# Kernel optimization log

Measured on AMD Instinct MI355X. Metric: run time of the kernel, lower is better.

Reference implementation:

```python
import jax, jax.numpy as jnp
import numpy as np

EPS = 1e-5

def _sage(x, src, dst, counts, w_msg, w_root, b, n_nodes):
    # mean-aggregate neighbor features (src -> dst), then linear
    msgs = x[src]                                             # [E, D]
    summed = jax.ops.segment_sum(msgs, dst, num_segments=n_nodes)
    mean = summed / counts                                    # [N, D]
    return mean @ w_msg + x @ w_root + b

def _layernorm(x, gamma, beta):
    mu = jnp.mean(x, axis=-1, keepdims=True)
    var = jnp.var(x, axis=-1, keepdims=True)
    return (x - mu) * jax.lax.rsqrt(var + EPS) * gamma + beta

def setup_inputs() -> dict:
    key = jax.random.key(0)
    N, E, D = 100000, 1600000, 128
    ks = jax.random.split(key, 20)
    z = jax.random.normal(ks[0], (N, D), dtype=jnp.float32)
    edge_index = jax.random.randint(ks[1], (2, E), 0, N, dtype=jnp.int32)
    def lin(k, din, dout):
        return jax.random.normal(k, (din, dout), dtype=jnp.float32) / np.sqrt(din)
    params = {
        'w_msg1': lin(ks[2], 128, 256), 'w_root1': lin(ks[3], 128, 256),
        'b1': jnp.zeros((256,), jnp.float32),
        'g1': jax.random.uniform(ks[4], (256,), jnp.float32, 0.9, 1.1),
        'beta1': jax.random.normal(ks[5], (256,), jnp.float32) * 0.05,
        'w_msg2': lin(ks[6], 256, 256), 'w_root2': lin(ks[7], 256, 256),
        'b2': jnp.zeros((256,), jnp.float32),
        'g2': jax.random.uniform(ks[8], (256,), jnp.float32, 0.9, 1.1),
        'beta2': jax.random.normal(ks[9], (256,), jnp.float32) * 0.05,
        'w_msg3': lin(ks[10], 256, 128), 'w_root3': lin(ks[11], 256, 128),
        'b3': jnp.zeros((128,), jnp.float32),
        'g3': jax.random.uniform(ks[12], (128,), jnp.float32, 0.9, 1.1),
        'beta3': jax.random.normal(ks[13], (128,), jnp.float32) * 0.05,
        'w_msg4': lin(ks[14], 128, 9), 'w_root4': lin(ks[15], 128, 9),
        'b4': jnp.zeros((9,), jnp.float32),
    }
    return {'z': z, 'edge_index': edge_index, **params}

def reference(z, edge_index,
              w_msg1, w_root1, b1, g1, beta1,
              w_msg2, w_root2, b2, g2, beta2,
              w_msg3, w_root3, b3, g3, beta3,
              w_msg4, w_root4, b4):
    N = z.shape[0]
    src, dst = edge_index[0], edge_index[1]
    counts = jax.ops.segment_sum(jnp.ones_like(dst, dtype=z.dtype), dst, num_segments=N)
    counts = jnp.maximum(counts, 1.0)[:, None]
    x = jax.nn.relu(_layernorm(_sage(z, src, dst, counts, w_msg1, w_root1, b1, N), g1, beta1))
    x = jax.nn.relu(_layernorm(_sage(x, src, dst, counts, w_msg2, w_root2, b2, N), g2, beta2))
    x = jax.nn.relu(_layernorm(_sage(x, src, dst, counts, w_msg3, w_root3, b3, N), g3, beta3))
    x = _sage(x, src, dst, counts, w_msg4, w_root4, b4, N)
    return x
```

## Files before the change

### kernel.cpp

```cpp
#include <hip/hip_runtime.h>
#include <hip/hip_bf16.h>


#define EPS 1e-5f

typedef unsigned short u16;
typedef short bf16x8_t __attribute__((ext_vector_type(8)));
typedef float f32x4_t __attribute__((ext_vector_type(4)));

__device__ inline unsigned int bfpack(float a, float b) {
    unsigned int ua = __builtin_bit_cast(unsigned int, a);
    unsigned int ub = __builtin_bit_cast(unsigned int, b);
    ua += 0x7fffu + ((ua >> 16) & 1u);
    ub += 0x7fffu + ((ub >> 16) & 1u);
    return (ua >> 16) | (ub & 0xffff0000u);
}

__device__ inline u16 bfr(float a) {
    unsigned int u = __builtin_bit_cast(unsigned int, a);
    u += 0x7fffu + ((u >> 16) & 1u);
    return (u16)(u >> 16);
}

__device__ inline float bf2f(u16 v) {
    unsigned int u = ((unsigned int)v) << 16;
    return __builtin_bit_cast(float, u);
}

__device__ inline float bflo(unsigned int q) { return __builtin_bit_cast(float, q << 16); }
__device__ inline float bfhi(unsigned int q) { return __builtin_bit_cast(float, q & 0xffff0000u); }

#define ACC8(A, Q)                                         \
    A[0] += bflo(Q.x); A[1] += bfhi(Q.x);                  \
    A[2] += bflo(Q.y); A[3] += bfhi(Q.y);                  \
    A[4] += bflo(Q.z); A[5] += bfhi(Q.z);                  \
    A[6] += bflo(Q.w); A[7] += bfhi(Q.w);

__global__ __launch_bounds__(256) void zero_f4(float4* __restrict__ p, int n4) {
    int i = blockIdx.x * 256 + threadIdx.x;
    if (i < n4) p[i] = make_float4(0.f, 0.f, 0.f, 0.f);
}

__global__ __launch_bounds__(256) void cast_bf16(const float* __restrict__ x,
                                                 u16* __restrict__ y, int n4) {
    int i = blockIdx.x * 256 + threadIdx.x;
    if (i >= n4) return;
    float4 v = ((const float4*)x)[i];
    ((uint2*)y)[i] = make_uint2(bfpack(v.x, v.y), bfpack(v.z, v.w));
}

struct WtJobs {
    const float* W[6];
    u16* WT[6];
    int K[6], N[6];
};
__global__ __launch_bounds__(256) void transpose_cast6(WtJobs jobs) {
    int j = blockIdx.y;
    int idx = blockIdx.x * 256 + threadIdx.x;
    int K = jobs.K[j], Nn = jobs.N[j];
    if (idx >= K * Nn) return;
    int k = idx / Nn, n = idx - k * Nn;
    jobs.WT[j][(long)n * K + k] = bfr(jobs.W[j][idx]);
}

__global__ __launch_bounds__(256) void count_deg(const int* __restrict__ dst,
                                                 int* __restrict__ deg, int E) {
    int e = blockIdx.x * 256 + threadIdx.x;
    if (e < E) atomicAdd(&deg[dst[e]], 1);
}

__global__ __launch_bounds__(256) void partial_sums(const int* __restrict__ deg,
                                                    int* __restrict__ partials, int N) {
    __shared__ int lds[4];
    int tid = threadIdx.x;
    int base = blockIdx.x * 1024 + tid * 4;
    int s = 0;
    if (base + 3 < N) {
        int4 v = *(const int4*)(deg + base);
        s = v.x + v.y + v.z + v.w;
    } else {
        for (int i = 0; i < 4; ++i)
            if (base + i < N) s += deg[base + i];
    }
#pragma unroll
    for (int m = 32; m >= 1; m >>= 1) s += __shfl_xor(s, m);
    if ((tid & 63) == 0) lds[tid >> 6] = s;
    __syncthreads();
    if (tid == 0) partials[blockIdx.x] = lds[0] + lds[1] + lds[2] + lds[3];
}

__global__ __launch_bounds__(256) void scan_partials(int* __restrict__ partials, int nb) {
    __shared__ int lds[256];
    int tid = threadIdx.x;
    int v = (tid < nb) ? partials[tid] : 0;
    lds[tid] = v;
    __syncthreads();
    for (int off = 1; off < 256; off <<= 1) {
        int t = (tid >= off) ? lds[tid - off] : 0;
        __syncthreads();
        lds[tid] += t;
        __syncthreads();
    }
    if (tid < nb) partials[tid] = lds[tid] - v;
}

__global__ __launch_bounds__(256) void write_rowptr(const int* __restrict__ deg,
                                                    const int* __restrict__ partials,
                                                    int* __restrict__ rowptr,
                                                    int* __restrict__ cursor,
                                                    float* __restrict__ inv, int N, int E) {
    __shared__ int lds[256];
    int tid = threadIdx.x;
    int base = blockIdx.x * 1024 + tid * 4;
    int d[4];
    int s = 0;
#pragma unroll
    for (int i = 0; i < 4; ++i) {
        d[i] = (base + i < N) ? deg[base + i] : 0;
        s += d[i];
    }
    lds[tid] = s;
    __syncthreads();
    for (int off = 1; off < 256; off <<= 1) {
        int t = (tid >= off) ? lds[tid - off] : 0;
        __syncthreads();
        lds[tid] += t;
        __syncthreads();
    }
    int run = partials[blockIdx.x] + lds[tid] - s;
#pragma unroll
    for (int i = 0; i < 4; ++i) {
        int idx = base + i;
        if (idx < N) {
            rowptr[idx] = run;
            cursor[idx] = run;
            inv[idx] = 1.0f / fmaxf((float)d[i], 1.0f);
            run += d[i];
        }
    }
    if (blockIdx.x == 0 && tid == 0) rowptr[N] = E;
}

__global__ __launch_bounds__(256) void fill_csr_range(const int* __restrict__ src,
                                                      const int* __restrict__ dst,
                                                      int* __restrict__ cursor,
                                                      int* __restrict__ eidx, int E,
                                                      int lo, int bs) {
    int e = blockIdx.x * 256 + threadIdx.x;
    if (e >= E) return;
    int d = dst[e];
    if ((unsigned)(d - lo) < (unsigned)bs) {
        int p = atomicAdd(&cursor[d], 1);
        eidx[p] = src[e];
    }
}

__global__ __launch_bounds__(256) void gather_scale256(const u16* __restrict__ x,
                                                       const int* __restrict__ rowptr,
                                                       const int* __restrict__ eidx,
                                                       const float* __restrict__ inv,
                                                       u16* __restrict__ agg, int N) {
    int wave = threadIdx.x >> 6;
    int lane = threadIdx.x & 63;
    int half = lane >> 5;
    int sub = lane & 31;
    int row = blockIdx.x * 4 + wave;
    if (row >= N) return;
    int beg = rowptr[row], end = rowptr[row + 1];
    float a[8] = {}, b[8] = {};
    int j = beg + half;
    for (; j + 2 < end; j += 4) {
        uint4 q0 = *(const uint4*)(x + (long)eidx[j] * 256 + sub * 8);
        uint4 q1 = *(const uint4*)(x + (long)eidx[j + 2] * 256 + sub * 8);
        ACC8(a, q0);
        ACC8(b, q1);
    }
    if (j < end) {
        uint4 q = *(const uint4*)(x + (long)eidx[j] * 256 + sub * 8);
        ACC8(a, q);
    }
#pragma unroll
    for (int i = 0; i < 8; ++i) {
        a[i] += b[i];
        a[i] += __shfl_xor(a[i], 32);
    }
    if (half == 0) {
        float s = inv[row];
        uint4 o;
        o.x = bfpack(a[0] * s, a[1] * s);
        o.y = bfpack(a[2] * s, a[3] * s);
        o.z = bfpack(a[4] * s, a[5] * s);
        o.w = bfpack(a[6] * s, a[7] * s);
        *(uint4*)(agg + (long)row * 256 + sub * 8) = o;
    }
}

__global__ __launch_bounds__(256) void gather_scale128(const u16* __restrict__ x,
                                                       const int* __restrict__ rowptr,
                                                       const int* __restrict__ eidx,
                                                       const float* __restrict__ inv,
                                                       u16* __restrict__ agg, int N) {
    int wave = threadIdx.x >> 6;
    int lane = threadIdx.x & 63;
    int quarter = lane >> 4;
    int sub = lane & 15;
    int row = blockIdx.x * 4 + wave;
    if (row >= N) return;
    int beg = rowptr[row], end = rowptr[row + 1];
    float a[8] = {}, b[8] = {};
    int j = beg + quarter;
    for (; j + 4 < end; j += 8) {
        uint4 q0 = *(const uint4*)(x + (long)eidx[j] * 128 + sub * 8);
        uint4 q1 = *(const uint4*)(x + (long)eidx[j + 4] * 128 + sub * 8);
        ACC8(a, q0);
        ACC8(b, q1);
    }
    if (j < end) {
        uint4 q = *(const uint4*)(x + (long)eidx[j] * 128 + sub * 8);
        ACC8(a, q);
    }
#pragma unroll
    for (int i = 0; i < 8; ++i) {
        a[i] += b[i];
        a[i] += __shfl_xor(a[i], 16);
        a[i] += __shfl_xor(a[i], 32);
    }
    if (quarter == 0) {
        float s = inv[row];
        uint4 o;
        o.x = bfpack(a[0] * s, a[1] * s);
        o.y = bfpack(a[2] * s, a[3] * s);
        o.z = bfpack(a[4] * s, a[5] * s);
        o.w = bfpack(a[6] * s, a[7] * s);
        *(uint4*)(agg + (long)row * 128 + sub * 8) = o;
    }
}

__global__ __launch_bounds__(256) void gather_add_ln_relu128(const u16* __restrict__ y,
                                                             const int* __restrict__ rowptr,
                                                             const int* __restrict__ eidx,
                                                             const float* __restrict__ inv,
                                                             const u16* __restrict__ r,
                                                             const float* __restrict__ g,
                                                             const float* __restrict__ be,
                                                             u16* __restrict__ out, int N) {
    int wave = threadIdx.x >> 6;
    int lane = threadIdx.x & 63;
    int quarter = lane >> 4;
    int sub = lane & 15;
    int row = blockIdx.x * 4 + wave;
    if (row >= N) return;
    int beg = rowptr[row], end = rowptr[row + 1];
    float a[8] = {}, b[8] = {};
    int j = beg + quarter;
    for (; j + 4 < end; j += 8) {
        uint4 q0 = *(const uint4*)(y + (long)eidx[j] * 128 + sub * 8);
        uint4 q1 = *(const uint4*)(y + (long)eidx[j + 4] * 128 + sub * 8);
        ACC8(a, q0);
        ACC8(b, q1);
    }
    if (j < end) {
        uint4 q = *(const uint4*)(y + (long)eidx[j] * 128 + sub * 8);
        ACC8(a, q);
    }
#pragma unroll
    for (int i = 0; i < 8; ++i) {
        a[i] += b[i];
        a[i] += __shfl_xor(a[i], 16);
        a[i] += __shfl_xor(a[i], 32);
    }
    float iv = inv[row];
    uint4 rr = *(const uint4*)(r + (long)row * 128 + sub * 8);
    float v[8];
    v[0] = a[0] * iv + bflo(rr.x); v[1] = a[1] * iv + bfhi(rr.x);
    v[2] = a[2] * iv + bflo(rr.y); v[3] = a[3] * iv + bfhi(rr.y);
    v[4] = a[4] * iv + bflo(rr.z); v[5] = a[5] * iv + bfhi(rr.z);
    v[6] = a[6] * iv + bflo(rr.w); v[7] = a[7] * iv + bfhi(rr.w);
    float s = 0.f, ss = 0.f;
#pragma unroll
    for (int i = 0; i < 8; ++i) { s += v[i]; ss += v[i] * v[i]; }
#pragma unroll
    for (int m = 8; m >= 1; m >>= 1) {
        s += __shfl_xor(s, m);
        ss += __shfl_xor(ss, m);
    }
    float mean = s / 128.f;
    float var = ss / 128.f - mean * mean;
    float rs = rsqrtf(var + EPS);
    if (quarter == 0) {
        int col = sub * 8;
        float4 g0 = *(const float4*)&g[col];
        float4 g1 = *(const float4*)&g[col + 4];
        float4 e0 = *(const float4*)&be[col];
        float4 e1 = *(const float4*)&be[col + 4];
        float o0 = fmaxf((v[0] - mean) * rs * g0.x + e0.x, 0.f);
        float o1 = fmaxf((v[1] - mean) * rs * g0.y + e0.y, 0.f);
        float o2 = fmaxf((v[2] - mean) * rs * g0.z + e0.z, 0.f);
        float o3 = fmaxf((v[3] - mean) * rs * g0.w + e0.w, 0.f);
        float o4 = fmaxf((v[4] - mean) * rs * g1.x + e1.x, 0.f);
        float o5 = fmaxf((v[5] - mean) * rs * g1.y + e1.y, 0.f);
        float o6 = fmaxf((v[6] - mean) * rs * g1.z + e1.z, 0.f);
        float o7 = fmaxf((v[7] - mean) * rs * g1.w + e1.w, 0.f);
        uint4 o;
        o.x = bfpack(o0, o1);
        o.y = bfpack(o2, o3);
        o.z = bfpack(o4, o5);
        o.w = bfpack(o6, o7);
        *(uint4*)(out + (long)row * 128 + sub * 8) = o;
    }
}

__global__ __launch_bounds__(256) void gather9_final(const u16* __restrict__ y,
                                                     const int* __restrict__ rowptr,
                                                     const int* __restrict__ eidx,
                                                     const float* __restrict__ inv,
                                                     const float* __restrict__ r,
                                                     float* __restrict__ out, int N) {
    int idx = blockIdx.x * 256 + threadIdx.x;
    int row = idx >> 4;
    int c = idx & 15;
    if (row >= N || c >= 9) return;
    int beg = rowptr[row], end = rowptr[row + 1];
    float a = 0.f;
    for (int j = beg; j < end; ++j) a += bf2f(y[(long)eidx[j] * 9 + c]);
    out[(long)row * 9 + c] = a * inv[row] + r[(long)row * 9 + c];
}

__global__ __launch_bounds__(256) void mfma_gemm_wide_ln(const u16* A1,
                                                         const u16* __restrict__ A2,
                                                         const u16* __restrict__ WT1,
                                                         const u16* __restrict__ WT2,
                                                         const float* __restrict__ bias,
                                                         const float* __restrict__ g,
                                                         const float* __restrict__ be,
                                                         u16* out, int M, int K) {
    __shared__ __align__(16) u16 smem[64 * 260];
    u16* As = smem;
    u16* Ws = smem + 64 * 40;
    const int tid = threadIdx.x;
    const int bm = blockIdx.x * 64;
    const int l = tid & 63;
    const int w = tid >> 6;
    const int wr = (w & 1) * 32;
    const int wc = (w >> 1) * 128;
    const int ln15 = l & 15;
    const int quad = l >> 4;

    f32x4_t acc[2][8];
#pragma unroll
    for (int i = 0; i < 2; ++i)
#pragma unroll
        for (int j = 0; j < 8; ++j) acc[i][j] = (f32x4_t){0.f, 0.f, 0.f, 0.f};

    const int ar = tid >> 2;
    const int akh = (tid & 3) * 8;

    for (int pass = 0; pass < 2; ++pass) {
        const u16* A = pass ? A2 : A1;
        const u16* WT = pass ? WT2 : WT1;
        for (int k0 = 0; k0 < K; k0 += 32) {
            uint4 q0 = make_uint4(0, 0, 0, 0);
            int gr = bm + ar;
            if (gr < M) q0 = *(const uint4*)(A + (long)gr * K + k0 + akh);
            *(uint4*)(As + ar * 40 + akh) = q0;
            const u16* wp = WT + (long)tid * K + k0;
            *(uint4*)(Ws + tid * 40 + 0) = ((const uint4*)wp)[0];
            *(uint4*)(Ws + tid * 40 + 8) = ((const uint4*)wp)[1];
            *(uint4*)(Ws + tid * 40 + 16) = ((const uint4*)wp)[2];
            *(uint4*)(Ws + tid * 40 + 24) = ((const uint4*)wp)[3];
            __syncthreads();

            bf16x8_t a[2], b[8];
#pragma unroll
            for (int i = 0; i < 2; ++i)
                a[i] = *(const bf16x8_t*)(As + (wr + i * 16 + ln15) * 40 + quad * 8);
#pragma unroll
            for (int j = 0; j < 8; ++j)
                b[j] = *(const bf16x8_t*)(Ws + (wc + j * 16 + ln15) * 40 + quad * 8);
#pragma unroll
            for (int i = 0; i < 2; ++i)
#pragma unroll
                for (int j = 0; j < 8; ++j)
                    acc[i][j] = __builtin_amdgcn_mfma_f32_16x16x32_bf16(a[i], b[j], acc[i][j], 0, 0, 0);
            __syncthreads();
        }
    }

#pragma unroll
    for (int j = 0; j < 8; ++j) {
        int col = wc + j * 16 + ln15;
        float bv = bias[col];
#pragma unroll
        for (int i = 0; i < 2; ++i) {
            int row0 = wr + i * 16 + quad * 4;
            f32x4_t c = acc[i][j];
#pragma unroll
            for (int p = 0; p < 4; ++p) smem[(row0 + p) * 260 + col] = bfr(c[p] + bv);
        }
    }
    __syncthreads();

    float4 g4 = *(const float4*)&g[l * 4];
    float4 be4 = *(const float4*)&be[l * 4];
    for (int rr = 0; rr < 16; ++rr) {
        int lrow = w * 16 + rr;
        int grow = bm + lrow;
        if (grow >= M) break;
        ushort4 ld = *(const ushort4*)(smem + lrow * 260 + l * 4);
        float v0 = bf2f(ld.x), v1 = bf2f(ld.y), v2 = bf2f(ld.z), v3 = bf2f(ld.w);
        float s = v0 + v1 + v2 + v3;
        float ss = v0 * v0 + v1 * v1 + v2 * v2 + v3 * v3;
#pragma unroll
        for (int m = 32; m >= 1; m >>= 1) {
            s += __shfl_xor(s, m);
            ss += __shfl_xor(ss, m);
        }
        float mean = s / 256.f;
        float var = ss / 256.f - mean * mean;
        float rs = rsqrtf(var + EPS);
        v0 = fmaxf((v0 - mean) * rs * g4.x + be4.x, 0.f);
        v1 = fmaxf((v1 - mean) * rs * g4.y + be4.y, 0.f);
        v2 = fmaxf((v2 - mean) * rs * g4.z + be4.z, 0.f);
        v3 = fmaxf((v3 - mean) * rs * g4.w + be4.w, 0.f);
        ((uint2*)out)[(long)grow * 64 + l] = make_uint2(bfpack(v0, v1), bfpack(v2, v3));
    }
}

__global__ __launch_bounds__(256) void mfma_gemm_dual(const u16* __restrict__ A,
                                                      const u16* __restrict__ WTa,
                                                      const u16* __restrict__ WTb,
                                                      const float* __restrict__ biasb,
                                                      u16* __restrict__ outa,
                                                      u16* __restrict__ outb, int M, int K) {
    __shared__ u16 As[128 * 40];
    __shared__ u16 Ws[128 * 40];
    const u16* WT = blockIdx.y ? WTb : WTa;
    u16* out = blockIdx.y ? outb : outa;
    const float* bias = blockIdx.y ? biasb : nullptr;
    const int tid = threadIdx.x;
    const int bm = blockIdx.x * 128;
    const int l = tid & 63;
    const int w = tid >> 6;
    const int wr = (w & 1) * 64;
    const int wc = (w >> 1) * 64;
    const int ln15 = l & 15;
    const int quad = l >> 4;

    f32x4_t acc[4][4];
#pragma unroll
    for (int i = 0; i < 4; ++i)
#pragma unroll
        for (int j = 0; j < 4; ++j) acc[i][j] = (f32x4_t){0.f, 0.f, 0.f, 0.f};

    const int sr = tid >> 1;
    const int kh = (tid & 1) * 16;

    for (int k0 = 0; k0 < K; k0 += 32) {
        uint4 q0 = make_uint4(0, 0, 0, 0), q1 = make_uint4(0, 0, 0, 0);
        int gr = bm + sr;
        if (gr < M) {
            const u16* ap = A + (long)gr * K + k0 + kh;
            q0 = ((const uint4*)ap)[0];
            q1 = ((const uint4*)ap)[1];
        }
        *(uint4*)(As + sr * 40 + kh) = q0;
        *(uint4*)(As + sr * 40 + kh + 8) = q1;
        const u16* wp = WT + (long)sr * K + k0 + kh;
        *(uint4*)(Ws + sr * 40 + kh) = ((const uint4*)wp)[0];
        *(uint4*)(Ws + sr * 40 + kh + 8) = ((const uint4*)wp)[1];
        __syncthreads();

        bf16x8_t a[4], b[4];
#pragma unroll
        for (int i = 0; i < 4; ++i)
            a[i] = *(const bf16x8_t*)(As + (wr + i * 16 + ln15) * 40 + quad * 8);
#pragma unroll
        for (int j = 0; j < 4; ++j)
            b[j] = *(const bf16x8_t*)(Ws + (wc + j * 16 + ln15) * 40 + quad * 8);
#pragma unroll
        for (int i = 0; i < 4; ++i)
#pragma unroll
            for (int j = 0; j < 4; ++j)
                acc[i][j] = __builtin_amdgcn_mfma_f32_16x16x32_bf16(a[i], b[j], acc[i][j], 0, 0, 0);
        __syncthreads();
    }

#pragma unroll
    for (int j = 0; j < 4; ++j) {
        int col = wc + j * 16 + ln15;
        float bv = bias ? bias[col] : 0.f;
#pragma unroll
        for (int i = 0; i < 4; ++i) {
            int row0 = bm + wr + i * 16 + quad * 4;
            f32x4_t c = acc[i][j];
#pragma unroll
            for (int p = 0; p < 4; ++p) {
                int row = row0 + p;
                if (row < M) out[(long)row * 128 + col] = bfr(c[p] + bv);
            }
        }
    }
}

__global__ __launch_bounds__(320) void gemm4_bf(const u16* __restrict__ x,
                                                const float* __restrict__ wm,
                                                const float* __restrict__ wrt,
                                                const float* __restrict__ b,
                                                u16* __restrict__ y, float* __restrict__ r,
                                                int M) {
    __shared__ float xs[16][132];
    __shared__ float ws[128][20];
    int tid = threadIdx.x;
    int m0 = blockIdx.x * 16;
    for (int idx = tid; idx < 16 * 128; idx += 320) {
        int rr = idx >> 7, kk = idx & 127;
        int gm = m0 + rr;
        xs[rr][kk] = (gm < M) ? bf2f(x[(long)gm * 128 + kk]) : 0.f;
    }
    for (int idx = tid; idx < 128 * 18; idx += 320) {
        int kk = idx / 18, cc = idx % 18;
        ws[kk][cc] = (cc < 9) ? wm[kk * 9 + cc] : wrt[kk * 9 + cc - 9];
    }
    __syncthreads();
    if (tid < 288) {
        int rr = tid / 18, cc = tid % 18;
        float acc = 0.f;
#pragma unroll 8
        for (int kk = 0; kk < 128; ++kk) acc += xs[rr][kk] * ws[kk][cc];
        int gm = m0 + rr;
        if (gm < M) {
            if (cc < 9) y[(long)gm * 9 + cc] = bfr(acc);
            else r[(long)gm * 9 + cc - 9] = acc + b[cc - 9];
        }
    }
}

static inline int cdiv(long a, long b) { return (int)((a + b - 1) / b); }

extern "C" void kernel_launch(void* const* d_in, const int* in_sizes, int n_in,
                              void* d_out, int out_size, void* d_ws, size_t ws_size,
                              hipStream_t stream) {
    const int N = in_sizes[0] / 128;
    const int E = in_sizes[1] / 2;

    const float* z = (const float*)d_in[0];
    const int* ei = (const int*)d_in[1];
    const int* src = ei;
    const int* dstp = ei + E;
    const float* wm1 = (const float*)d_in[2];
    const float* wr1 = (const float*)d_in[3];
    const float* b1 = (const float*)d_in[4];
    const float* g1 = (const float*)d_in[5];
    const float* be1 = (const float*)d_in[6];
    const float* wm2 = (const float*)d_in[7];
    const float* wr2 = (const float*)d_in[8];
    const float* b2 = (const float*)d_in[9];
    const float* g2 = (const float*)d_in[10];
    const float* be2 = (const float*)d_in[11];
    const float* wm3 = (const float*)d_in[12];
    const float* wr3 = (const float*)d_in[13];
    const float* b3 = (const float*)d_in[14];
    const float* g3 = (const float*)d_in[15];
    const float* be3 = (const float*)d_in[16];
    const float* wm4 = (const float*)d_in[17];
    const float* wr4 = (const float*)d_in[18];
    const float* b4 = (const float*)d_in[19];
    float* out = (float*)d_out;

    u16* aggh2 = (u16*)d_ws;
    u16* h1b = aggh2 + (size_t)N * 256;
    u16* zb = h1b + (size_t)N * 256;
    u16* agg1 = zb + (size_t)N * 128;
    float* inv = (float*)(agg1 + (size_t)N * 128);
    int* deg = (int*)(inv + N);
    int* rowptr = deg + N + 4;
    int* cursor = rowptr + N + 4;
    int* partials = cursor + N + 4;
    int* eidx = partials + 256;
    u16* wt1m = (u16*)(eidx + E);
    u16* wt1r = wt1m + 256 * 128;
    u16* wt2m = wt1r + 256 * 128;
    u16* wt2r = wt2m + 256 * 256;
    u16* wt3m = wt2r + 256 * 256;
    u16* wt3r = wt3m + 128 * 256;

    u16* y3b = agg1;
    u16* r3b = zb;
    u16* h3b = h1b;
    u16* y4 = aggh2;
    float* r4 = (float*)(aggh2 + (size_t)N * 16);

    const int nscan = cdiv(N, 1024);

    cast_bf16<<<cdiv((long)N * 32, 256), 256, 0, stream>>>(z, zb, N * 32);
    zero_f4<<<cdiv(N, 1024), 256, 0, stream>>>((float4*)deg, cdiv(N, 4));
    count_deg<<<cdiv(E, 256), 256, 0, stream>>>(dstp, deg, E);
    partial_sums<<<nscan, 256, 0, stream>>>(deg, partials, N);
    scan_partials<<<1, 256, 0, stream>>>(partials, nscan);
    write_rowptr<<<nscan, 256, 0, stream>>>(deg, partials, rowptr, cursor, inv, N, E);
    {
        const int P = 4;
        int bs = cdiv(N, P);
        for (int b = 0; b < P; ++b)
            fill_csr_range<<<cdiv(E, 256), 256, 0, stream>>>(src, dstp, cursor, eidx, E,
                                                             b * bs, bs);
    }
    {
        WtJobs jobs;
        jobs.W[0] = wm1; jobs.WT[0] = wt1m; jobs.K[0] = 128; jobs.N[0] = 256;
        jobs.W[1] = wr1; jobs.WT[1] = wt1r; jobs.K[1] = 128; jobs.N[1] = 256;
        jobs.W[2] = wm2; jobs.WT[2] = wt2m; jobs.K[2] = 256; jobs.N[2] = 256;
        jobs.W[3] = wr2; jobs.WT[3] = wt2r; jobs.K[3] = 256; jobs.N[3] = 256;
        jobs.W[4] = wm3; jobs.WT[4] = wt3m; jobs.K[4] = 256; jobs.N[4] = 128;
        jobs.W[5] = wr3; jobs.WT[5] = wt3r; jobs.K[5] = 256; jobs.N[5] = 128;
        dim3 g(256, 6);
        transpose_cast6<<<g, 256, 0, stream>>>(jobs);
    }

    gather_scale128<<<cdiv(N, 4), 256, 0, stream>>>(zb, rowptr, eidx, inv, agg1, N);
    mfma_gemm_wide_ln<<<cdiv(N, 64), 256, 0, stream>>>(agg1, zb, wt1m, wt1r, b1, g1, be1,
                                                       h1b, N, 128);

    gather_scale256<<<cdiv(N, 4), 256, 0, stream>>>(h1b, rowptr, eidx, inv, aggh2, N);
    mfma_gemm_wide_ln<<<cdiv(N, 64), 256, 0, stream>>>(aggh2, h1b, wt2m, wt2r, b2, g2, be2,
                                                       aggh2, N, 256);

    {
        dim3 g(cdiv(N, 128), 2);
        mfma_gemm_dual<<<g, 256, 0, stream>>>(aggh2, wt3m, wt3r, b3, y3b, r3b, N, 256);
    }
    gather_add_ln_relu128<<<cdiv(N, 4), 256, 0, stream>>>(y3b, rowptr, eidx, inv, r3b, g3,
                                                          be3, h3b, N);

    gemm4_bf<<<cdiv(N, 16), 320, 0, stream>>>(h3b, wm4, wr4, b4, y4, r4, N);
    gather9_final<<<cdiv((long)N * 16, 256), 256, 0, stream>>>(y4, rowptr, eidx, inv, r4, out, N);
}
```

Measured before the change: 829.8 us.

## Enlarge fused GEMM+LayerNorm tile to 128 rows with register-resident LN

Replaces the 64-row wide GEMM+LayerNorm kernel with a 128-row tile in which each wave computes 64x128. The LayerNorm statistics are now reduced from the accumulator registers through shuffles and a small shared buffer, so the bf16 round trip through shared memory is gone. The output is no longer written in place, so buffers are re-mapped: h2 now goes to zb, and y3/r3 go to aggh2. The CSR fill pass count also drops from 4 to 2. The larger tile halves weight reloads per row and removes an intermediate rounding step, at the cost of more accumulator registers (possibly lower occupancy) and uncoalesced per-element output stores.

```diff
diff --git a/kernel.cpp b/kernel.cpp
--- a/kernel.cpp
+++ b/kernel.cpp
@@ -326,43 +326,49 @@
     out[(long)row * 9 + c] = a * inv[row] + r[(long)row * 9 + c];
 }
 
-__global__ __launch_bounds__(256) void mfma_gemm_wide_ln(const u16* A1,
-                                                         const u16* __restrict__ A2,
-                                                         const u16* __restrict__ WT1,
-                                                         const u16* __restrict__ WT2,
-                                                         const float* __restrict__ bias,
-                                                         const float* __restrict__ g,
-                                                         const float* __restrict__ be,
-                                                         u16* out, int M, int K) {
-    __shared__ __align__(16) u16 smem[64 * 260];
-    u16* As = smem;
-    u16* Ws = smem + 64 * 40;
+__global__ __launch_bounds__(256) void mfma_gemm128_ln(const u16* __restrict__ A1,
+                                                       const u16* __restrict__ A2,
+                                                       const u16* __restrict__ WT1,
+                                                       const u16* __restrict__ WT2,
+                                                       const float* __restrict__ bias,
+                                                       const float* __restrict__ g,
+                                                       const float* __restrict__ be,
+                                                       u16* __restrict__ out, int M, int K) {
+    __shared__ u16 As[128 * 40];
+    __shared__ u16 Ws[256 * 40];
+    __shared__ float sred[128][2];
+    __shared__ float ssred[128][2];
     const int tid = threadIdx.x;
-    const int bm = blockIdx.x * 64;
+    const int bm = blockIdx.x * 128;
     const int l = tid & 63;
     const int w = tid >> 6;
-    const int wr = (w & 1) * 32;
+    const int wr = (w & 1) * 64;
     const int wc = (w >> 1) * 128;
     const int ln15 = l & 15;
     const int quad = l >> 4;
 
-    f32x4_t acc[2][8];
-#pragma unroll
-    for (int i = 0; i < 2; ++i)
+    f32x4_t acc[4][8];
+#pragma unroll
+    for (int i = 0; i < 4; ++i)
 #pragma unroll
         for (int j = 0; j < 8; ++j) acc[i][j] = (f32x4_t){0.f, 0.f, 0.f, 0.f};
 
-    const int ar = tid >> 2;
-    const int akh = (tid & 3) * 8;
+    const int sr = tid >> 1;
+    const int kh = (tid & 1) * 16;
 
     for (int pass = 0; pass < 2; ++pass) {
         const u16* A = pass ? A2 : A1;
         const u16* WT = pass ? WT2 : WT1;
         for (int k0 = 0; k0 < K; k0 += 32) {
-            uint4 q0 = make_uint4(0, 0, 0, 0);
-            int gr = bm + ar;
-            if (gr < M) q0 = *(const uint4*)(A + (long)gr * K + k0 + akh);
-            *(uint4*)(As + ar * 40 + akh) = q0;
+            uint4 q0 = make_uint4(0, 0, 0, 0), q1 = make_uint4(0, 0, 0, 0);
+            int gr = bm + sr;
+            if (gr < M) {
+                const u16* ap = A + (long)gr * K + k0 + kh;
+                q0 = ((const uint4*)ap)[0];
+                q1 = ((const uint4*)ap)[1];
+            }
+            *(uint4*)(As + sr * 40 + kh) = q0;
+            *(uint4*)(As + sr * 40 + kh + 8) = q1;
             const u16* wp = WT + (long)tid * K + k0;
             *(uint4*)(Ws + tid * 40 + 0) = ((const uint4*)wp)[0];
             *(uint4*)(Ws + tid * 40 + 8) = ((const uint4*)wp)[1];
@@ -370,15 +376,15 @@
             *(uint4*)(Ws + tid * 40 + 24) = ((const uint4*)wp)[3];
             __syncthreads();
 
-            bf16x8_t a[2], b[8];
-#pragma unroll
-            for (int i = 0; i < 2; ++i)
+            bf16x8_t a[4], b[8];
+#pragma unroll
+            for (int i = 0; i < 4; ++i)
                 a[i] = *(const bf16x8_t*)(As + (wr + i * 16 + ln15) * 40 + quad * 8);
 #pragma unroll
             for (int j = 0; j < 8; ++j)
                 b[j] = *(const bf16x8_t*)(Ws + (wc + j * 16 + ln15) * 40 + quad * 8);
 #pragma unroll
-            for (int i = 0; i < 2; ++i)
+            for (int i = 0; i < 4; ++i)
 #pragma unroll
                 for (int j = 0; j < 8; ++j)
                     acc[i][j] = __builtin_amdgcn_mfma_f32_16x16x32_bf16(a[i], b[j], acc[i][j], 0, 0, 0);
@@ -386,43 +392,69 @@
         }
     }
 
+    float bv[8];
+#pragma unroll
+    for (int j = 0; j < 8; ++j) bv[j] = bias[wc + j * 16 + ln15];
+#pragma unroll
+    for (int i = 0; i < 4; ++i)
+#pragma unroll
+        for (int j = 0; j < 8; ++j)
+#pragma unroll
+            for (int p = 0; p < 4; ++p) acc[i][j][p] += bv[j];
+
+#pragma unroll
+    for (int i = 0; i < 4; ++i) {
+        float s[4] = {}, ss[4] = {};
+#pragma unroll
+        for (int j = 0; j < 8; ++j)
+#pragma unroll
+            for (int p = 0; p < 4; ++p) {
+                float x = acc[i][j][p];
+                s[p] += x;
+                ss[p] += x * x;
+            }
+#pragma unroll
+        for (int m = 1; m <= 8; m <<= 1)
+#pragma unroll
+            for (int p = 0; p < 4; ++p) {
+                s[p] += __shfl_xor(s[p], m);
+                ss[p] += __shfl_xor(ss[p], m);
+            }
+        if (ln15 == 0) {
+#pragma unroll
+            for (int p = 0; p < 4; ++p) {
+                int r = wr + i * 16 + quad * 4 + p;
+                sred[r][w >> 1] = s[p];
+                ssred[r][w >> 1] = ss[p];
+            }
+        }
+    }
+    __syncthreads();
+
+    float gv[8], ev[8];
 #pragma unroll
     for (int j = 0; j < 8; ++j) {
-        int col = wc + j * 16 + ln15;
-        float bv = bias[col];
-#pragma unroll
-        for (int i = 0; i < 2; ++i) {
-            int row0 = wr + i * 16 + quad * 4;
-            f32x4_t c = acc[i][j];
-#pragma unroll
-            for (int p = 0; p < 4; ++p) smem[(row0 + p) * 260 + col] = bfr(c[p] + bv);
+        gv[j] = g[wc + j * 16 + ln15];
+        ev[j] = be[wc + j * 16 + ln15];
+    }
+#pragma unroll
+    for (int i = 0; i < 4; ++i) {
+#pragma unroll
+        for (int p = 0; p < 4; ++p) {
+            int r = wr + i * 16 + quad * 4 + p;
+            int grow = bm + r;
+            if (grow >= M) continue;
+            float s = sred[r][0] + sred[r][1];
+            float ss = ssred[r][0] + ssred[r][1];
+            float mean = s / 256.f;
+            float var = ss / 256.f - mean * mean;
+            float rs = rsqrtf(var + EPS);
+#pragma unroll
+            for (int j = 0; j < 8; ++j) {
+                float y = (acc[i][j][p] - mean) * rs * gv[j] + ev[j];
+                out[(long)grow * 256 + wc + j * 16 + ln15] = bfr(fmaxf(y, 0.f));
+            }
         }
-    }
-    __syncthreads();
-
-    float4 g4 = *(const float4*)&g[l * 4];
-    float4 be4 = *(const float4*)&be[l * 4];
-    for (int rr = 0; rr < 16; ++rr) {
-        int lrow = w * 16 + rr;
-        int grow = bm + lrow;
-        if (grow >= M) break;
-        ushort4 ld = *(const ushort4*)(smem + lrow * 260 + l * 4);
-        float v0 = bf2f(ld.x), v1 = bf2f(ld.y), v2 = bf2f(ld.z), v3 = bf2f(ld.w);
-        float s = v0 + v1 + v2 + v3;
-        float ss = v0 * v0 + v1 * v1 + v2 * v2 + v3 * v3;
-#pragma unroll
-        for (int m = 32; m >= 1; m >>= 1) {
-            s += __shfl_xor(s, m);
-            ss += __shfl_xor(ss, m);
-        }
-        float mean = s / 256.f;
-        float var = ss / 256.f - mean * mean;
-        float rs = rsqrtf(var + EPS);
-        v0 = fmaxf((v0 - mean) * rs * g4.x + be4.x, 0.f);
-        v1 = fmaxf((v1 - mean) * rs * g4.y + be4.y, 0.f);
-        v2 = fmaxf((v2 - mean) * rs * g4.z + be4.z, 0.f);
-        v3 = fmaxf((v3 - mean) * rs * g4.w + be4.w, 0.f);
-        ((uint2*)out)[(long)grow * 64 + l] = make_uint2(bfpack(v0, v1), bfpack(v2, v3));
     }
 }
 
@@ -584,8 +616,9 @@
     u16* wt3m = wt2r + 256 * 256;
     u16* wt3r = wt3m + 128 * 256;
 
-    u16* y3b = agg1;
-    u16* r3b = zb;
+    u16* h2 = zb;
+    u16* y3b = aggh2;
+    u16* r3b = aggh2 + (size_t)N * 128;
     u16* h3b = h1b;
     u16* y4 = aggh2;
     float* r4 = (float*)(aggh2 + (size_t)N * 16);
@@ -599,7 +632,7 @@
     scan_partials<<<1, 256, 0, stream>>>(partials, nscan);
     write_rowptr<<<nscan, 256, 0, stream>>>(deg, partials, rowptr, cursor, inv, N, E);
     {
-        const int P = 4;
+        const int P = 2;
         int bs = cdiv(N, P);
         for (int b = 0; b < P; ++b)
             fill_csr_range<<<cdiv(E, 256), 256, 0, stream>>>(src, dstp, cursor, eidx, E,
@@ -618,16 +651,16 @@
     }
 
     gather_scale128<<<cdiv(N, 4), 256, 0, stream>>>(zb, rowptr, eidx, inv, agg1, N);
-    mfma_gemm_wide_ln<<<cdiv(N, 64), 256, 0, stream>>>(agg1, zb, wt1m, wt1r, b1, g1, be1,
-                                                       h1b, N, 128);
+    mfma_gemm128_ln<<<cdiv(N, 128), 256, 0, stream>>>(agg1, zb, wt1m, wt1r, b1, g1, be1,
+                                                      h1b, N, 128);
 
     gather_scale256<<<cdiv(N, 4), 256, 0, stream>>>(h1b, rowptr, eidx, inv, aggh2, N);
-    mfma_gemm_wide_ln<<<cdiv(N, 64), 256, 0, stream>>>(aggh2, h1b, wt2m, wt2r, b2, g2, be2,
-                                                       aggh2, N, 256);
+    mfma_gemm128_ln<<<cdiv(N, 128), 256, 0, stream>>>(aggh2, h1b, wt2m, wt2r, b2, g2, be2,
+                                                      h2, N, 256);
 
     {
         dim3 g(cdiv(N, 128), 2);
-        mfma_gemm_dual<<<g, 256, 0, stream>>>(aggh2, wt3m, wt3r, b3, y3b, r3b, N, 256);
+        mfma_gemm_dual<<<g, 256, 0, stream>>>(h2, wt3m, wt3r, b3, y3b, r3b, N, 256);
     }
     gather_add_ln_relu128<<<cdiv(N, 4), 256, 0, stream>>>(y3b, rowptr, eidx, inv, r3b, g3,
                                                           be3, h3b, N);
```

Result: slower. 864.8 us (+4.2%).
